# Performance work log

Measured on AMD Instinct MI355X. Metric: run time of the kernel, lower is better.

The kernel has to match this reference:

```python
import jax, jax.numpy as jnp
import numpy as np
from jax import lax

N_INPUT, N_HIDDEN, N_OUTPUT = 1024, 2048, 1024
T, B = 512, 64

def setup_inputs() -> dict:
    key = jax.random.key(0)
    k_x, k_ih, k_hh, k_out = jax.random.split(key, 4)
    stdv = 1.0 / np.sqrt(N_HIDDEN)
    xs = jax.random.normal(k_x, (T, B, N_INPUT), dtype=jnp.float32)
    # torch nn.Linear weights are [out_features, in_features], init U(-stdv, stdv)
    W_ih = jax.random.uniform(k_ih, (N_HIDDEN, N_INPUT), jnp.float32, -stdv, stdv)
    W_hh = jax.random.uniform(k_hh, (N_HIDDEN, N_HIDDEN), jnp.float32, -stdv, stdv)
    W_out = jax.random.uniform(k_out, (N_OUTPUT, N_HIDDEN), jnp.float32, -stdv, stdv)
    return {"xs": xs, "W_ih": W_ih, "W_hh": W_hh, "W_out": W_out}

def reference(xs, W_ih, W_hh, W_out):
    # xs: [T, B, n_input] time-major. state starts as None -> relu(W_ih x),
    # which equals relu(W_ih x + W_hh * 0), so h0 = zeros is exact.
    n_hidden = W_hh.shape[0]
    h0 = jnp.zeros((xs.shape[1], n_hidden), dtype=xs.dtype)

    def step(h, x):
        h = jax.nn.relu(x @ W_ih.T + h @ W_hh.T)  # [B, n_hidden]
        return h, h

    _, h_seq = lax.scan(step, h0, xs)        # [T, B, n_hidden]
    ys = h_seq @ W_out.T                     # [T, B, n_output]
    return jnp.transpose(ys, (1, 0, 2))      # [B, T, n_output] (transpose(0,1))
```

## Files before the change

kernel.cpp:

```cpp
#include <hip/hip_runtime.h>
#include <hip/hip_bf16.h>
#include <stdint.h>


#define TT 512
#define BB 64
#define NIN 1024
#define NH 2048
#define NOUT 1024

typedef __attribute__((ext_vector_type(8))) short bf8;
typedef __attribute__((ext_vector_type(4))) float f4;
typedef __attribute__((ext_vector_type(4))) unsigned int u4;

static __device__ __forceinline__ unsigned short f2bf(float f) {
  __hip_bfloat16 h = __float2bfloat16(f);
  return __builtin_bit_cast(unsigned short, h);
}
static __device__ __forceinline__ float bf2f(unsigned short v) {
  return __bfloat162float(__builtin_bit_cast(__hip_bfloat16, v));
}
static __device__ __forceinline__ u4 pack8(const float* f) {
  u4 r;
#pragma unroll
  for (int i = 0; i < 4; ++i) {
    unsigned lo = f2bf(f[2 * i]);
    unsigned hi = f2bf(f[2 * i + 1]);
    r[i] = lo | (hi << 16);
  }
  return r;
}

static __device__ __forceinline__ size_t sl_idx(int m, int col) {
  return ((((size_t)(m >> 6) * 4 + ((m & 63) >> 4)) * 64 + (col >> 5)) << 9) +
         (size_t)((m & 63) & 15) * 32 + (col & 31);
}

template <bool ABF, bool TRANS>
__global__ void gemm_bt(const void* __restrict__ Av, const float* __restrict__ Bw,
                        void* __restrict__ Cv, int M, int N, int K) {
  constexpr int BM = 128, BN = 128, BK = 32;
  __shared__ u4 As[BM * 4];
  __shared__ u4 Bs[BN * 4];
  const int nt = N / BN;
  const int mi = (int)blockIdx.x / nt;
  const int ni = (int)blockIdx.x % nt;
  const int m0 = mi * BM, n0 = ni * BN;
  const int t = threadIdx.x;
  const int l = t & 63, w = t >> 6, wr = w >> 1, wc = w & 1;
  const int lr = l & 15, lq = l >> 4;

  f4 acc[4][4] = {};

  const int srow = t >> 1;
  const int sc0 = (t & 1) * 2;

  for (int kt = 0; kt < K; kt += BK) {
    if (ABF) {
      const unsigned short* A = (const unsigned short*)Av;
#pragma unroll
      for (int cc = 0; cc < 2; ++cc) {
        int c = sc0 + cc;
        u4 v = *(const u4*)(A + sl_idx(m0 + srow, kt + c * 8));
        As[srow * 4 + (c ^ ((srow ^ (srow >> 2)) & 3))] = v;
      }
    } else {
      const float* A = (const float*)Av;
#pragma unroll
      for (int cc = 0; cc < 2; ++cc) {
        int c = sc0 + cc;
        const float* p = A + (size_t)(m0 + srow) * K + kt + c * 8;
        float4 v0 = *(const float4*)p;
        float4 v1 = *(const float4*)(p + 4);
        float f[8] = {v0.x, v0.y, v0.z, v0.w, v1.x, v1.y, v1.z, v1.w};
        As[srow * 4 + (c ^ ((srow ^ (srow >> 2)) & 3))] = pack8(f);
      }
    }
#pragma unroll
    for (int cc = 0; cc < 2; ++cc) {
      int c = sc0 + cc;
      const float* p = Bw + (size_t)(n0 + srow) * K + kt + c * 8;
      float4 v0 = *(const float4*)p;
      float4 v1 = *(const float4*)(p + 4);
      float f[8] = {v0.x, v0.y, v0.z, v0.w, v1.x, v1.y, v1.z, v1.w};
      Bs[srow * 4 + (c ^ ((srow ^ (srow >> 2)) & 3))] = pack8(f);
    }
    __syncthreads();

    bf8 a[4], b[4];
#pragma unroll
    for (int i = 0; i < 4; ++i) {
      int ra = wr * 64 + i * 16 + lr;
      a[i] = __builtin_bit_cast(bf8, As[ra * 4 + (lq ^ ((ra ^ (ra >> 2)) & 3))]);
      int rb = wc * 64 + i * 16 + lr;
      b[i] = __builtin_bit_cast(bf8, Bs[rb * 4 + (lq ^ ((rb ^ (rb >> 2)) & 3))]);
    }
#pragma unroll
    for (int i = 0; i < 4; ++i)
#pragma unroll
      for (int j = 0; j < 4; ++j)
        acc[i][j] = __builtin_amdgcn_mfma_f32_16x16x32_bf16(a[i], b[j], acc[i][j], 0, 0, 0);
    __syncthreads();
  }

  if (TRANS) {
    float* C = (float*)Cv;
#pragma unroll
    for (int i = 0; i < 4; ++i)
#pragma unroll
      for (int j = 0; j < 4; ++j)
#pragma unroll
        for (int r = 0; r < 4; ++r) {
          int m = m0 + wr * 64 + i * 16 + lq * 4 + r;
          int n = n0 + wc * 64 + j * 16 + lr;
          C[(size_t)(m & 63) * (TT * NOUT) + (size_t)(m >> 6) * NOUT + n] = acc[i][j][r];
        }
  } else {
    unsigned short* C = (unsigned short*)Cv;
#pragma unroll
    for (int i = 0; i < 4; ++i)
#pragma unroll
      for (int j = 0; j < 4; ++j)
#pragma unroll
        for (int r = 0; r < 4; ++r) {
          int m = m0 + wr * 64 + i * 16 + lq * 4 + r;
          int n = n0 + wc * 64 + j * 16 + lr;
          C[sl_idx(m, n)] = f2bf(acc[i][j][r]);
        }
  }
}

__global__ __launch_bounds__(512, 2) void rnn_recur(unsigned short* __restrict__ hseq,
                                                    const float* __restrict__ Whh,
                                                    unsigned* __restrict__ flags) {
  __shared__ u4 Wl[32 * 256];
  __shared__ float red[2][4][16][36];
  const int t = threadIdx.x;
  const int bid = (int)blockIdx.x;
  const int g = (bid & 7) >> 1;
  const int jb = ((bid >> 3) << 1) | (bid & 1);
  const int j0 = jb * 32;

  {
    const int jl = t >> 4;
    const int ci = t & 15;
#pragma unroll
    for (int q = 0; q < 16; ++q) {
      int cc = ci * 16 + q;
      const float* p = Whh + (size_t)(j0 + jl) * NH + cc * 8;
      float4 v0 = *(const float4*)p;
      float4 v1 = *(const float4*)(p + 4);
      float f[8] = {v0.x, v0.y, v0.z, v0.w, v1.x, v1.y, v1.z, v1.w};
      Wl[jl * 256 + (cc ^ (jl & 7))] = pack8(f);
    }
  }

  const int l = t & 63, w = t >> 6;
  const int lr = l & 15, lq = l >> 4;
  const int kg = w >> 1, jh = w & 1;

  char* hb = (char*)hseq;
  const size_t gofs = (size_t)g << 16;

  const int wr_r = l >> 2;
  const int wjq = l & 3;
  const size_t wbyte = (size_t)wr_r * 64 + jh * 32 + wjq * 8;

  unsigned long long pre = 0;

  __syncthreads();

  if (w < 2) {
    size_t e0 = (gofs + ((size_t)jb << 10)) + wbyte;
    unsigned long long p0 = __hip_atomic_load((const unsigned long long*)(hb + e0),
                                              __ATOMIC_RELAXED, __HIP_MEMORY_SCOPE_AGENT);
    unsigned long long hv = 0;
#pragma unroll
    for (int i = 0; i < 4; ++i) {
      unsigned long long x = (p0 >> (16 * i)) & 0xffffull;
      if (!(x & 0x8000ull)) hv |= x << (16 * i);
    }
    __hip_atomic_store((unsigned long long*)(hb + e0), hv, __ATOMIC_RELAXED,
                       __HIP_MEMORY_SCOPE_AGENT);
    asm volatile("s_waitcnt vmcnt(0)" ::: "memory");
    if (l == 0)
      __hip_atomic_store(flags + ((g * 64 + jb) * 2 + w), 1u, __ATOMIC_RELAXED,
                         __HIP_MEMORY_SCOPE_AGENT);
    pre = __hip_atomic_load(
        (const unsigned long long*)(hb + ((size_t)(1 * 4) << 16) + gofs + ((size_t)jb << 10) + wbyte),
        __ATOMIC_RELAXED, __HIP_MEMORY_SCOPE_AGENT);
  }

  for (int ts = 1; ts < TT; ++ts) {
    {
      const unsigned* fp = flags + ((g * 64 + kg * 16 + (l >> 1)) * 2 + (l & 1));
      long spins = 0;
      for (;;) {
        unsigned fv = (l < 32) ? __hip_atomic_load(fp, __ATOMIC_RELAXED,
                                                   __HIP_MEMORY_SCOPE_AGENT)
                               : 0xffffffffu;
        if (__ballot(fv >= (unsigned)ts) == ~0ull) break;
        __builtin_amdgcn_s_sleep(1);
        if (++spins > (1L << 22)) break;
      }
    }
    asm volatile("" ::: "memory");

    const size_t rowoff = (size_t)(l & 15) * 64 + (size_t)(l >> 4) * 16;
    const size_t base = (((size_t)(ts - 1) * 4) << 16) + gofs + ((size_t)(kg * 16) << 10) + rowoff;
    unsigned long long a0 = (unsigned long long)(uintptr_t)(hb + base);
    unsigned long long a1 = a0 + 4096;
    unsigned long long a2 = a0 + 8192;
    unsigned long long a3 = a0 + 12288;
    u4 av[16];
    asm volatile(
        "global_load_dwordx4 %0, %16, off sc0 sc1\n\t"
        "global_load_dwordx4 %1, %16, off offset:1024 sc0 sc1\n\t"
        "global_load_dwordx4 %2, %16, off offset:2048 sc0 sc1\n\t"
        "global_load_dwordx4 %3, %16, off offset:3072 sc0 sc1\n\t"
        "global_load_dwordx4 %4, %17, off sc0 sc1\n\t"
        "global_load_dwordx4 %5, %17, off offset:1024 sc0 sc1\n\t"
        "global_load_dwordx4 %6, %17, off offset:2048 sc0 sc1\n\t"
        "global_load_dwordx4 %7, %17, off offset:3072 sc0 sc1\n\t"
        "global_load_dwordx4 %8, %18, off sc0 sc1\n\t"
        "global_load_dwordx4 %9, %18, off offset:1024 sc0 sc1\n\t"
        "global_load_dwordx4 %10, %18, off offset:2048 sc0 sc1\n\t"
        "global_load_dwordx4 %11, %18, off offset:3072 sc0 sc1\n\t"
        "global_load_dwordx4 %12, %19, off sc0 sc1\n\t"
        "global_load_dwordx4 %13, %19, off offset:1024 sc0 sc1\n\t"
        "global_load_dwordx4 %14, %19, off offset:2048 sc0 sc1\n\t"
        "global_load_dwordx4 %15, %19, off offset:3072 sc0 sc1\n\t"
        "s_waitcnt vmcnt(0)"
        : "=&v"(av[0]), "=&v"(av[1]), "=&v"(av[2]), "=&v"(av[3]),
          "=&v"(av[4]), "=&v"(av[5]), "=&v"(av[6]), "=&v"(av[7]),
          "=&v"(av[8]), "=&v"(av[9]), "=&v"(av[10]), "=&v"(av[11]),
          "=&v"(av[12]), "=&v"(av[13]), "=&v"(av[14]), "=&v"(av[15])
        : "v"(a0), "v"(a1), "v"(a2), "v"(a3)
        : "memory");

    f4 acc0 = {}, acc1 = {};
#pragma unroll
    for (int c = 0; c < 16; ++c) {
      bf8 af = __builtin_bit_cast(bf8, av[c]);
      int ci = kg * 64 + c * 4 + lq;
      bf8 bfr = __builtin_bit_cast(bf8, Wl[(jh * 16 + lr) * 256 + (ci ^ (lr & 7))]);
      if (c & 1)
        acc1 = __builtin_amdgcn_mfma_f32_16x16x32_bf16(af, bfr, acc1, 0, 0, 0);
      else
        acc0 = __builtin_amdgcn_mfma_f32_16x16x32_bf16(af, bfr, acc0, 0, 0, 0);
    }
    f4 a2v = acc0 + acc1;

    const int buf = ts & 1;
#pragma unroll
    for (int i = 0; i < 4; ++i) red[buf][kg][(l >> 4) * 4 + i][jh * 16 + (l & 15)] = a2v[i];
    __syncthreads();

    if (w < 2) {
      __builtin_amdgcn_s_setprio(1);
      f4 s = {};
#pragma unroll
      for (int q = 0; q < 4; ++q) s += *(const f4*)&red[buf][q][wr_r][jh * 16 + wjq * 4];
      float sf[4];
#pragma unroll
      for (int i = 0; i < 4; ++i) {
        float v = s[i] + bf2f((unsigned short)((pre >> (16 * i)) & 0xffffull));
        sf[i] = v > 0.f ? v : 0.f;
      }
      unsigned lo = (unsigned)f2bf(sf[0]) | ((unsigned)f2bf(sf[1]) << 16);
      unsigned hi = (unsigned)f2bf(sf[2]) | ((unsigned)f2bf(sf[3]) << 16);
      unsigned long long hv = (unsigned long long)lo | ((unsigned long long)hi << 32);
      size_t eo = (((size_t)ts * 4) << 16) + gofs + ((size_t)jb << 10) + wbyte;
      __hip_atomic_store((unsigned long long*)(hb + eo), hv, __ATOMIC_RELAXED,
                         __HIP_MEMORY_SCOPE_AGENT);
      asm volatile("s_waitcnt vmcnt(0)" ::: "memory");
      if (l == 0)
        __hip_atomic_store(flags + ((g * 64 + jb) * 2 + w), (unsigned)(ts + 1),
                           __ATOMIC_RELAXED, __HIP_MEMORY_SCOPE_AGENT);
      if (ts + 1 < TT)
        pre = __hip_atomic_load(
            (const unsigned long long*)(hb + (((size_t)(ts + 1) * 4) << 16) + gofs +
                                        ((size_t)jb << 10) + wbyte),
            __ATOMIC_RELAXED, __HIP_MEMORY_SCOPE_AGENT);
      __builtin_amdgcn_s_setprio(0);
    }
  }
}

__global__ void kinit(unsigned* f) { f[threadIdx.x] = 0u; }

extern "C" void kernel_launch(void* const* d_in, const int* in_sizes, int n_in,
                              void* d_out, int out_size, void* d_ws, size_t ws_size,
                              hipStream_t stream) {
  const float* xs = (const float*)d_in[0];
  const float* Wih = (const float*)d_in[1];
  const float* Whh = (const float*)d_in[2];
  const float* Wout = (const float*)d_in[3];

  unsigned short* hseq = (unsigned short*)d_ws;
  unsigned* flags = (unsigned*)((char*)d_ws + (size_t)TT * BB * NH * 2);

  kinit<<<1, 512, 0, stream>>>(flags);

  gemm_bt<false, false><<<(TT * BB / 128) * (NH / 128), 256, 0, stream>>>(
      (const void*)xs, Wih, (void*)hseq, TT * BB, NH, NIN);

  rnn_recur<<<256, 512, 0, stream>>>(hseq, Whh, flags);

  gemm_bt<true, true><<<(TT * BB / 128) * (NOUT / 128), 256, 0, stream>>>(
      (const void*)hseq, Wout, d_out, TT * BB, NOUT, NH);
}
```

Measured before the change: 3.946 ms.

## Use sign-bit as per-element ready tag and drop store waitcnt in recurrence

```diff
diff --git a/kernel.cpp b/kernel.cpp
--- a/kernel.cpp
+++ b/kernel.cpp
@@ -38,7 +38,8 @@
 
 template <bool ABF, bool TRANS>
 __global__ void gemm_bt(const void* __restrict__ Av, const float* __restrict__ Bw,
-                        void* __restrict__ Cv, int M, int N, int K) {
+                        void* __restrict__ Cv, unsigned char* __restrict__ plane,
+                        int M, int N, int K) {
   constexpr int BM = 128, BN = 128, BK = 32;
   __shared__ u4 As[BM * 4];
   __shared__ u4 Bs[BN * 4];
@@ -54,6 +55,7 @@
 
   const int srow = t >> 1;
   const int sc0 = (t & 1) * 2;
+  const u4 msk = {0x7fff7fffu, 0x7fff7fffu, 0x7fff7fffu, 0x7fff7fffu};
 
   for (int kt = 0; kt < K; kt += BK) {
     if (ABF) {
@@ -62,6 +64,7 @@
       for (int cc = 0; cc < 2; ++cc) {
         int c = sc0 + cc;
         u4 v = *(const u4*)(A + sl_idx(m0 + srow, kt + c * 8));
+        v &= msk;
         As[srow * 4 + (c ^ ((srow ^ (srow >> 2)) & 3))] = v;
       }
     } else {
@@ -125,12 +128,18 @@
         for (int r = 0; r < 4; ++r) {
           int m = m0 + wr * 64 + i * 16 + lq * 4 + r;
           int n = n0 + wc * 64 + j * 16 + lr;
-          C[sl_idx(m, n)] = f2bf(acc[i][j][r]);
+          unsigned short v = f2bf(acc[i][j][r]);
+          size_t sl = sl_idx(m, n);
+          C[sl] = (unsigned short)(v & 0x7fffu);
+          unsigned long long bal = __ballot((v & 0x8000u) != 0);
+          if ((l & 7) == 0)
+            plane[sl >> 3] = (unsigned char)((bal >> (l & ~7)) & 0xffull);
         }
   }
 }
 
 __global__ __launch_bounds__(512, 2) void rnn_recur(unsigned short* __restrict__ hseq,
+                                                    const unsigned char* __restrict__ plane,
                                                     const float* __restrict__ Whh,
                                                     unsigned* __restrict__ flags) {
   __shared__ u4 Wl[32 * 256];
@@ -161,34 +170,35 @@
 
   char* hb = (char*)hseq;
   const size_t gofs = (size_t)g << 16;
+  const u4 msk = {0x7fff7fffu, 0x7fff7fffu, 0x7fff7fffu, 0x7fff7fffu};
 
   const int wr_r = l >> 2;
   const int wjq = l & 3;
   const size_t wbyte = (size_t)wr_r * 64 + jh * 32 + wjq * 8;
 
   unsigned long long pre = 0;
+  unsigned nib = 0;
 
   __syncthreads();
 
   if (w < 2) {
-    size_t e0 = (gofs + ((size_t)jb << 10)) + wbyte;
+    size_t e0 = gofs + ((size_t)jb << 10) + wbyte;
     unsigned long long p0 = __hip_atomic_load((const unsigned long long*)(hb + e0),
                                               __ATOMIC_RELAXED, __HIP_MEMORY_SCOPE_AGENT);
-    unsigned long long hv = 0;
-#pragma unroll
-    for (int i = 0; i < 4; ++i) {
-      unsigned long long x = (p0 >> (16 * i)) & 0xffffull;
-      if (!(x & 0x8000ull)) hv |= x << (16 * i);
-    }
+    unsigned nib0 = (plane[e0 >> 4] >> (((e0 >> 3) & 1) * 4)) & 0xfu;
+    unsigned long long hv = 0x8000800080008000ull;
+#pragma unroll
+    for (int i = 0; i < 4; ++i)
+      if (!((nib0 >> i) & 1u)) hv |= ((p0 >> (16 * i)) & 0x7fffull) << (16 * i);
     __hip_atomic_store((unsigned long long*)(hb + e0), hv, __ATOMIC_RELAXED,
                        __HIP_MEMORY_SCOPE_AGENT);
-    asm volatile("s_waitcnt vmcnt(0)" ::: "memory");
     if (l == 0)
       __hip_atomic_store(flags + ((g * 64 + jb) * 2 + w), 1u, __ATOMIC_RELAXED,
                          __HIP_MEMORY_SCOPE_AGENT);
-    pre = __hip_atomic_load(
-        (const unsigned long long*)(hb + ((size_t)(1 * 4) << 16) + gofs + ((size_t)jb << 10) + wbyte),
-        __ATOMIC_RELAXED, __HIP_MEMORY_SCOPE_AGENT);
+    size_t e1 = ((size_t)4 << 16) + gofs + ((size_t)jb << 10) + wbyte;
+    pre = __hip_atomic_load((const unsigned long long*)(hb + e1), __ATOMIC_RELAXED,
+                            __HIP_MEMORY_SCOPE_AGENT);
+    nib = (plane[e1 >> 4] >> (((e1 >> 3) & 1) * 4)) & 0xfu;
   }
 
   for (int ts = 1; ts < TT; ++ts) {
@@ -207,41 +217,55 @@
     asm volatile("" ::: "memory");
 
     const size_t rowoff = (size_t)(l & 15) * 64 + (size_t)(l >> 4) * 16;
-    const size_t base = (((size_t)(ts - 1) * 4) << 16) + gofs + ((size_t)(kg * 16) << 10) + rowoff;
+    const size_t base =
+        (((size_t)(ts - 1) * 4) << 16) + gofs + ((size_t)(kg * 16) << 10) + rowoff;
     unsigned long long a0 = (unsigned long long)(uintptr_t)(hb + base);
     unsigned long long a1 = a0 + 4096;
     unsigned long long a2 = a0 + 8192;
     unsigned long long a3 = a0 + 12288;
     u4 av[16];
-    asm volatile(
-        "global_load_dwordx4 %0, %16, off sc0 sc1\n\t"
-        "global_load_dwordx4 %1, %16, off offset:1024 sc0 sc1\n\t"
-        "global_load_dwordx4 %2, %16, off offset:2048 sc0 sc1\n\t"
-        "global_load_dwordx4 %3, %16, off offset:3072 sc0 sc1\n\t"
-        "global_load_dwordx4 %4, %17, off sc0 sc1\n\t"
-        "global_load_dwordx4 %5, %17, off offset:1024 sc0 sc1\n\t"
-        "global_load_dwordx4 %6, %17, off offset:2048 sc0 sc1\n\t"
-        "global_load_dwordx4 %7, %17, off offset:3072 sc0 sc1\n\t"
-        "global_load_dwordx4 %8, %18, off sc0 sc1\n\t"
-        "global_load_dwordx4 %9, %18, off offset:1024 sc0 sc1\n\t"
-        "global_load_dwordx4 %10, %18, off offset:2048 sc0 sc1\n\t"
-        "global_load_dwordx4 %11, %18, off offset:3072 sc0 sc1\n\t"
-        "global_load_dwordx4 %12, %19, off sc0 sc1\n\t"
-        "global_load_dwordx4 %13, %19, off offset:1024 sc0 sc1\n\t"
-        "global_load_dwordx4 %14, %19, off offset:2048 sc0 sc1\n\t"
-        "global_load_dwordx4 %15, %19, off offset:3072 sc0 sc1\n\t"
-        "s_waitcnt vmcnt(0)"
-        : "=&v"(av[0]), "=&v"(av[1]), "=&v"(av[2]), "=&v"(av[3]),
-          "=&v"(av[4]), "=&v"(av[5]), "=&v"(av[6]), "=&v"(av[7]),
-          "=&v"(av[8]), "=&v"(av[9]), "=&v"(av[10]), "=&v"(av[11]),
-          "=&v"(av[12]), "=&v"(av[13]), "=&v"(av[14]), "=&v"(av[15])
-        : "v"(a0), "v"(a1), "v"(a2), "v"(a3)
-        : "memory");
+    int att = 0;
+    for (;;) {
+      asm volatile(
+          "global_load_dwordx4 %0, %16, off sc0 sc1\n\t"
+          "global_load_dwordx4 %1, %16, off offset:1024 sc0 sc1\n\t"
+          "global_load_dwordx4 %2, %16, off offset:2048 sc0 sc1\n\t"
+          "global_load_dwordx4 %3, %16, off offset:3072 sc0 sc1\n\t"
+          "global_load_dwordx4 %4, %17, off sc0 sc1\n\t"
+          "global_load_dwordx4 %5, %17, off offset:1024 sc0 sc1\n\t"
+          "global_load_dwordx4 %6, %17, off offset:2048 sc0 sc1\n\t"
+          "global_load_dwordx4 %7, %17, off offset:3072 sc0 sc1\n\t"
+          "global_load_dwordx4 %8, %18, off sc0 sc1\n\t"
+          "global_load_dwordx4 %9, %18, off offset:1024 sc0 sc1\n\t"
+          "global_load_dwordx4 %10, %18, off offset:2048 sc0 sc1\n\t"
+          "global_load_dwordx4 %11, %18, off offset:3072 sc0 sc1\n\t"
+          "global_load_dwordx4 %12, %19, off sc0 sc1\n\t"
+          "global_load_dwordx4 %13, %19, off offset:1024 sc0 sc1\n\t"
+          "global_load_dwordx4 %14, %19, off offset:2048 sc0 sc1\n\t"
+          "global_load_dwordx4 %15, %19, off offset:3072 sc0 sc1\n\t"
+          "s_waitcnt vmcnt(0)"
+          : "=&v"(av[0]), "=&v"(av[1]), "=&v"(av[2]), "=&v"(av[3]),
+            "=&v"(av[4]), "=&v"(av[5]), "=&v"(av[6]), "=&v"(av[7]),
+            "=&v"(av[8]), "=&v"(av[9]), "=&v"(av[10]), "=&v"(av[11]),
+            "=&v"(av[12]), "=&v"(av[13]), "=&v"(av[14]), "=&v"(av[15])
+          : "v"(a0), "v"(a1), "v"(a2), "v"(a3)
+          : "memory");
+      unsigned am = 0xffffffffu;
+#pragma unroll
+      for (int c = 0; c < 16; ++c)
+#pragma unroll
+        for (int d = 0; d < 4; ++d) am &= av[c][d];
+      bool ok = (am & 0x80008000u) == 0x80008000u;
+      if (__ballot(ok) == ~0ull) break;
+      __builtin_amdgcn_s_sleep(1);
+      if (++att > (1 << 20)) break;
+    }
 
     f4 acc0 = {}, acc1 = {};
 #pragma unroll
     for (int c = 0; c < 16; ++c) {
-      bf8 af = __builtin_bit_cast(bf8, av[c]);
+      u4 v = av[c] & msk;
+      bf8 af = __builtin_bit_cast(bf8, v);
       int ci = kg * 64 + c * 4 + lq;
       bf8 bfr = __builtin_bit_cast(bf8, Wl[(jh * 16 + lr) * 256 + (ci ^ (lr & 7))]);
       if (c & 1)
@@ -258,30 +282,35 @@
 
     if (w < 2) {
       __builtin_amdgcn_s_setprio(1);
+      float pf[4];
+#pragma unroll
+      for (int i = 0; i < 4; ++i) {
+        unsigned pv = (unsigned)((pre >> (16 * i)) & 0xffffull);
+        pv |= ((nib >> i) & 1u) << 15;
+        pf[i] = bf2f((unsigned short)pv);
+      }
       f4 s = {};
 #pragma unroll
       for (int q = 0; q < 4; ++q) s += *(const f4*)&red[buf][q][wr_r][jh * 16 + wjq * 4];
-      float sf[4];
+      unsigned long long hv = 0;
 #pragma unroll
       for (int i = 0; i < 4; ++i) {
-        float v = s[i] + bf2f((unsigned short)((pre >> (16 * i)) & 0xffffull));
-        sf[i] = v > 0.f ? v : 0.f;
-      }
-      unsigned lo = (unsigned)f2bf(sf[0]) | ((unsigned)f2bf(sf[1]) << 16);
-      unsigned hi = (unsigned)f2bf(sf[2]) | ((unsigned)f2bf(sf[3]) << 16);
-      unsigned long long hv = (unsigned long long)lo | ((unsigned long long)hi << 32);
+        float v = s[i] + pf[i];
+        v = v > 0.f ? v : 0.f;
+        hv |= (unsigned long long)(unsigned short)(f2bf(v) | 0x8000u) << (16 * i);
+      }
       size_t eo = (((size_t)ts * 4) << 16) + gofs + ((size_t)jb << 10) + wbyte;
       __hip_atomic_store((unsigned long long*)(hb + eo), hv, __ATOMIC_RELAXED,
                          __HIP_MEMORY_SCOPE_AGENT);
-      asm volatile("s_waitcnt vmcnt(0)" ::: "memory");
       if (l == 0)
         __hip_atomic_store(flags + ((g * 64 + jb) * 2 + w), (unsigned)(ts + 1),
                            __ATOMIC_RELAXED, __HIP_MEMORY_SCOPE_AGENT);
-      if (ts + 1 < TT)
-        pre = __hip_atomic_load(
-            (const unsigned long long*)(hb + (((size_t)(ts + 1) * 4) << 16) + gofs +
-                                        ((size_t)jb << 10) + wbyte),
-            __ATOMIC_RELAXED, __HIP_MEMORY_SCOPE_AGENT);
+      if (ts + 1 < TT) {
+        size_t en = (((size_t)(ts + 1) * 4) << 16) + gofs + ((size_t)jb << 10) + wbyte;
+        pre = __hip_atomic_load((const unsigned long long*)(hb + en), __ATOMIC_RELAXED,
+                                __HIP_MEMORY_SCOPE_AGENT);
+        nib = (plane[en >> 4] >> (((en >> 3) & 1) * 4)) & 0xfu;
+      }
       __builtin_amdgcn_s_setprio(0);
     }
   }
@@ -298,15 +327,16 @@
   const float* Wout = (const float*)d_in[3];
 
   unsigned short* hseq = (unsigned short*)d_ws;
-  unsigned* flags = (unsigned*)((char*)d_ws + (size_t)TT * BB * NH * 2);
+  unsigned char* plane = (unsigned char*)d_ws + ((size_t)TT * BB * NH * 2);
+  unsigned* flags = (unsigned*)(plane + ((size_t)TT * BB * NH / 8));
 
   kinit<<<1, 512, 0, stream>>>(flags);
 
   gemm_bt<false, false><<<(TT * BB / 128) * (NH / 128), 256, 0, stream>>>(
-      (const void*)xs, Wih, (void*)hseq, TT * BB, NH, NIN);
-
-  rnn_recur<<<256, 512, 0, stream>>>(hseq, Whh, flags);
+      (const void*)xs, Wih, (void*)hseq, plane, TT * BB, NH, NIN);
+
+  rnn_recur<<<256, 512, 0, stream>>>(hseq, plane, Whh, flags);
 
   gemm_bt<true, true><<<(TT * BB / 128) * (NOUT / 128), 256, 0, stream>>>(
-      (const void*)hseq, Wout, d_out, TT * BB, NOUT, NH);
-}
+      (const void*)hseq, Wout, d_out, plane, TT * BB, NOUT, NH);
+}
```

After: 3.848 ms (median of 2 runs). 2.5% less time.
